# Kernel optimization log

Hardware: AMD Instinct MI355X
Metric: run time of the kernel (lower is better)

## Reference

```python
import jax, jax.numpy as jnp
import numpy as np

B, T, S, H, D = 2, 2048, 2048, 16, 64
E = H * D  # embed_dim = 1024


def setup_inputs() -> dict:
    key = jax.random.key(0)
    k1, k2, k3, k4 = jax.random.split(key, 4)
    q = jax.random.normal(k1, (B, T, H, D), jnp.float32)
    kv = jax.random.normal(k2, (B, S, 2, H, D), jnp.float32)
    # nn.MultiheadAttention packed in-projection (xavier-ish scale) and out-projection
    in_proj_w = jax.random.normal(k3, (3 * E, E), jnp.float32) * (1.0 / np.sqrt(E)).astype(np.float32)
    in_proj_b = jnp.zeros((3 * E,), jnp.float32)
    out_proj_w = jax.random.normal(k4, (E, E), jnp.float32) * (1.0 / np.sqrt(E)).astype(np.float32)
    out_proj_b = jnp.zeros((E,), jnp.float32)
    return {"q": q, "kv": kv, "in_proj_w": in_proj_w, "in_proj_b": in_proj_b,
            "out_proj_w": out_proj_w, "out_proj_b": out_proj_b}


def reference(q, kv, in_proj_w, in_proj_b, out_proj_w, out_proj_b):
    Bq, Tq, Hh, Dd = q.shape
    Ss = kv.shape[1]
    Ee = Hh * Dd
    # flatten heads: q -> (B,T,E); kv unbinds k (two=0) and v (two=1)
    qf = q.reshape(Bq, Tq, Ee)
    kf = kv[:, :, 0].reshape(Bq, Ss, Ee)
    vf = kv[:, :, 1].reshape(Bq, Ss, Ee)
    wq, wk, wv = jnp.split(in_proj_w, 3, axis=0)
    bq, bk, bv = jnp.split(in_proj_b, 3)
    qp = (qf @ wq.T + bq).reshape(Bq, Tq, Hh, Dd).transpose(0, 2, 1, 3)  # bhtd
    kp = (kf @ wk.T + bk).reshape(Bq, Ss, Hh, Dd).transpose(0, 2, 1, 3)  # bhsd
    vp = (vf @ wv.T + bv).reshape(Bq, Ss, Hh, Dd).transpose(0, 2, 1, 3)  # bhsd
    scale = 1.0 / jnp.sqrt(jnp.asarray(Dd, qp.dtype))
    scores = jnp.einsum('bhtd,bhsd->bhts', qp, kp) * scale
    attn = jax.nn.softmax(scores, axis=-1)  # full SxS materialization, as in non-fused MHA
    ctx = jnp.einsum('bhts,bhsd->bhtd', attn, vp)
    ctx = ctx.transpose(0, 2, 1, 3).reshape(Bq, Tq, Ee)
    out = (ctx @ out_proj_w.T + out_proj_b).reshape(Bq, Tq, Hh, Dd)
    # need_weights=True default: weights averaged over heads -> (B,T,S)
    attn_weights = attn.mean(axis=1)
    return out, attn_weights
```

## Files before the change

kernel.cpp:

```cpp
#include <hip/hip_runtime.h>
#include <math.h>

#define Bb 2
#define Tt 2048
#define Ssz 2048
#define Hh 16
#define Dd 64
#define Ee 1024

#define NQ  (Bb*Tt*Ee)
#define NKV (Bb*Ssz*Ee)
#define NW  (3*Ee*Ee)
#define NWO (Ee*Ee)

#define LOG2E 1.44269504088896f

typedef __bf16 bf16x8 __attribute__((ext_vector_type(8)));
typedef float  floatx4 __attribute__((ext_vector_type(4)));
typedef unsigned short u16;
typedef unsigned int   u32;

__device__ __forceinline__ u16 f2bf(float f) {
    __bf16 h = (__bf16)f;
    union { __bf16 h; u16 u; } v; v.h = h; return v.u;
}
__device__ __forceinline__ float bf2f(u16 b) {
    union { u32 u; float f; } v; v.u = ((u32)b) << 16; return v.f;
}
__device__ __forceinline__ float load_f(const void* p, int i, bool isbf) {
    if (isbf) return bf2f(((const u16*)p)[i]);
    return ((const float*)p)[i];
}
__device__ __forceinline__ u32 load2(const void* p, int i, bool isbf) {
    if (isbf) return ((const u32*)p)[i >> 1];
    float2 f = ((const float2*)p)[i >> 1];
    return (u32)f2bf(f.x) | ((u32)f2bf(f.y) << 16);
}

typedef __attribute__((address_space(1))) const unsigned int gas_u32;
typedef __attribute__((address_space(3))) unsigned int las_u32;
__device__ __forceinline__ void gl_lds16(const u16* g, u16* l) {
    __builtin_amdgcn_global_load_lds((gas_u32*)g, (las_u32*)l, 16, 0, 0);
}

__device__ __forceinline__ int swz(int k, int row) {
    return (k & ~63) | ((((k >> 3) ^ row) & 7) << 3) | (k & 7);
}

__global__ void k_detect(const u32* __restrict__ qw, int* __restrict__ flag) {
    __shared__ int cnt;
    if (threadIdx.x == 0) cnt = 0;
    __syncthreads();
    int h = 0;
    for (int i = threadIdx.x; i < 4096; i += 256) {
        u32 w = qw[i];
        u32 b = (w >> 8) & 0x7Fu;
        if ((b & 0x7Cu) == 0x3Cu) h++;
    }
    atomicAdd(&cnt, h);
    __syncthreads();
    if (threadIdx.x == 0) flag[0] = (cnt > 2048) ? 1 : 0;
}

__global__ void k_pack(const void* __restrict__ q, const void* __restrict__ kv,
                       const void* __restrict__ w_in, const void* __restrict__ b_in,
                       const void* __restrict__ w_out, const void* __restrict__ b_out,
                       const int* __restrict__ flag,
                       u32* __restrict__ qb, u32* __restrict__ kb, u32* __restrict__ vb,
                       u32* __restrict__ wb, u32* __restrict__ wob, float* __restrict__ biases) {
    bool isbf = flag[0] != 0;
    int i = (blockIdx.x * 256 + threadIdx.x) * 2;
    if (i < NQ) { int row = i >> 10, k = i & 1023;
        qb[(((size_t)row << 10) | (u32)swz(k, row)) >> 1] = load2(q, i, isbf); return; }
    i -= NQ;
    if (i < NKV) { int row = i >> 10, e = i & 1023;
        kb[(((size_t)row << 10) | (u32)swz(e, row)) >> 1] = load2(kv, row*2048 + e, isbf); return; }
    i -= NKV;
    if (i < NKV) { int row = i >> 10, e = i & 1023;
        vb[(((size_t)row << 10) | (u32)swz(e, row)) >> 1] = load2(kv, row*2048 + 1024 + e, isbf); return; }
    i -= NKV;
    if (i < NW) { int row = i >> 10, k = i & 1023;
        wb[(((size_t)row << 10) | (u32)swz(k, row)) >> 1] = load2(w_in, i, isbf); return; }
    i -= NW;
    if (i < NWO) { int row = i >> 10, k = i & 1023;
        wob[(((size_t)row << 10) | (u32)swz(k, row)) >> 1] = load2(w_out, i, isbf); return; }
    i -= NWO;
    if (i < 3072) { biases[i] = load_f(b_in, i, isbf); biases[i+1] = load_f(b_in, i+1, isbf); return; }
    i -= 3072;
    if (i < 1024) { biases[3072+i] = load_f(b_out, i, isbf); biases[3072+i+1] = load_f(b_out, i+1, isbf); }
}

__device__ __forceinline__ void gemm128(const u16* __restrict__ Ab, const u16* __restrict__ Wb,
                                        u16* As, u16* Ws, floatx4 (&acc)[4][4], int tid) {
    int lane = tid & 63, w = tid >> 6, q = lane >> 4, ml = lane & 15;
    int mh = (w >> 1) * 64, nh = (w & 1) * 64;
    int rs = tid >> 3, cs = (tid & 7) * 8;
    for (int k0 = 0; k0 < 1024; k0 += 64) {
        __syncthreads();
#pragma unroll
        for (int j = 0; j < 4; ++j)
            gl_lds16(Ab + (size_t)(j*32 + rs) * 1024 + k0 + cs, &As[(j*32 + rs)*64 + cs]);
#pragma unroll
        for (int j = 0; j < 4; ++j)
            gl_lds16(Wb + (size_t)(j*32 + rs) * 1024 + k0 + cs, &Ws[(j*32 + rs)*64 + cs]);
        __syncthreads();
#pragma unroll
        for (int kk = 0; kk < 2; ++kk) {
            int gs = (((kk*4 + q) ^ ml) & 7) * 8;
            bf16x8 af[4], bfv[4];
#pragma unroll
            for (int mt = 0; mt < 4; ++mt) af[mt]  = *(const bf16x8*)&As[(mh + mt*16 + ml)*64 + gs];
#pragma unroll
            for (int nt = 0; nt < 4; ++nt) bfv[nt] = *(const bf16x8*)&Ws[(nh + nt*16 + ml)*64 + gs];
#pragma unroll
            for (int mt = 0; mt < 4; ++mt)
#pragma unroll
                for (int nt = 0; nt < 4; ++nt)
                    acc[mt][nt] = __builtin_amdgcn_mfma_f32_16x16x32_bf16(af[mt], bfv[nt], acc[mt][nt], 0, 0, 0);
        }
    }
}

__global__ __launch_bounds__(256) void k_gemm_qkv(const u16* __restrict__ qb, const u16* __restrict__ kb,
                                                  const u16* __restrict__ vb, const u16* __restrict__ wb,
                                                  const float* __restrict__ biases,
                                                  u16* __restrict__ Qp, u16* __restrict__ Kp,
                                                  u16* __restrict__ Vt) {
    __shared__ u16 As[128 * 64];
    __shared__ u16 Ws[128 * 64];
    int mode = blockIdx.z;
    const u16* A = (mode == 0) ? qb : (mode == 1) ? kb : vb;
    const u16* W = wb + (size_t)mode * Ee * Ee;
    const float* bias = biases + mode * 1024;
    int n0 = blockIdx.x * 128, m0 = blockIdx.y * 128;
    int tid = threadIdx.x, lane = tid & 63;
    int w = tid >> 6, q = lane >> 4, ml = lane & 15;
    int mh = (w >> 1) * 64, nh = (w & 1) * 64;

    floatx4 acc[4][4];
#pragma unroll
    for (int a = 0; a < 4; ++a)
#pragma unroll
        for (int b2 = 0; b2 < 4; ++b2) acc[a][b2] = (floatx4){0.f, 0.f, 0.f, 0.f};

    gemm128(A + (size_t)m0 * 1024, W + (size_t)n0 * 1024, As, Ws, acc, tid);

#pragma unroll
    for (int mt = 0; mt < 4; ++mt) {
#pragma unroll
        for (int nt = 0; nt < 4; ++nt) {
#pragma unroll
            for (int rg = 0; rg < 4; ++rg) {
                int m = m0 + mh + mt*16 + q*4 + rg;
                int n = n0 + nh + nt*16 + ml;
                float val = acc[mt][nt][rg] + bias[n];
                int b = m >> 11, t = m & 2047, hh = n >> 6, d = n & 63;
                if (mode == 0) {
                    int dsw = ((((d >> 3) ^ t) & 7) << 3) | (d & 7);
                    Qp[((size_t)(b*16 + hh) * 2048 + t) * 64 + dsw] = f2bf(val * (0.125f * LOG2E));
                } else if (mode == 1) {
                    int dsw = ((((d >> 3) ^ t) & 7) << 3) | (d & 7);
                    Kp[((size_t)(b*16 + hh) * 2048 + t) * 64 + dsw] = f2bf(val);
                } else {
                    int tsw = (t & ~63) | ((((t >> 3) ^ d) & 7) << 3) | (t & 7);
                    Vt[((size_t)(b*16 + hh) * 64 + d) * 2048 + tsw] = f2bf(val);
                }
            }
        }
    }
}

__global__ __launch_bounds__(256) void k_gemm_out(const u16* __restrict__ A, const u16* __restrict__ W,
                                                  const float* __restrict__ bias, void* __restrict__ Cout,
                                                  const int* __restrict__ flag) {
    __shared__ u16 As[128 * 64];
    __shared__ u16 Ws[128 * 64];
    int n0 = blockIdx.x * 128, m0 = blockIdx.y * 128;
    int tid = threadIdx.x, lane = tid & 63;
    int w = tid >> 6, q = lane >> 4, ml = lane & 15;
    int mh = (w >> 1) * 64, nh = (w & 1) * 64;

    floatx4 acc[4][4];
#pragma unroll
    for (int a = 0; a < 4; ++a)
#pragma unroll
        for (int b2 = 0; b2 < 4; ++b2) acc[a][b2] = (floatx4){0.f, 0.f, 0.f, 0.f};

    gemm128(A + (size_t)m0 * 1024, W + (size_t)n0 * 1024, As, Ws, acc, tid);

    bool outbf = flag[0] != 0;
#pragma unroll
    for (int mt = 0; mt < 4; ++mt) {
#pragma unroll
        for (int nt = 0; nt < 4; ++nt) {
#pragma unroll
            for (int rg = 0; rg < 4; ++rg) {
                int m = m0 + mh + mt*16 + q*4 + rg;
                int n = n0 + nh + nt*16 + ml;
                float val = acc[mt][nt][rg] + bias[n];
                if (outbf) ((u16*)Cout)[(size_t)m * 1024 + n] = f2bf(val);
                else       ((float*)Cout)[(size_t)m * 1024 + n] = val;
            }
        }
    }
}

__global__ __launch_bounds__(256) void k_flash(const u16* __restrict__ Qp, const u16* __restrict__ Kp,
                                               const u16* __restrict__ Vt, u16* __restrict__ ctx,
                                               float* __restrict__ lbuf) {
    __shared__ u16 Qs[128 * 64];
    __shared__ u16 Ks[64 * 64];
    __shared__ u16 Vs[64 * 64];
    __shared__ u16 Ps[128 * 64];
    int t0 = blockIdx.x * 128;
    int h  = blockIdx.y;
    int b  = blockIdx.z;
    const u16* Qh = Qp + (size_t)(b*16 + h) * 2048 * 64;
    const u16* Kh = Kp + (size_t)(b*16 + h) * 2048 * 64;
    const u16* Vh = Vt + (size_t)(b*16 + h) * 64 * 2048;
    int tid = threadIdx.x, lane = tid & 63;
    int w = tid >> 6, q = lane >> 4, ml = lane & 15;
    int rsw = tid >> 3, cs = (tid & 7) * 8;

#pragma unroll
    for (int j = 0; j < 4; ++j)
        gl_lds16(Qh + (size_t)(t0 + j*32 + rsw) * 64 + cs, &Qs[(j*32 + rsw)*64 + cs]);
    __syncthreads();

    bf16x8 qf[2][2];
#pragma unroll
    for (int mt = 0; mt < 2; ++mt)
#pragma unroll
        for (int kk = 0; kk < 2; ++kk)
            qf[mt][kk] = *(const bf16x8*)&Qs[(mt*64 + w*16 + ml)*64 + (((kk*4 + q) ^ ml) & 7)*8];

    float lp[2][4] = {{0.f,0.f,0.f,0.f},{0.f,0.f,0.f,0.f}};
    floatx4 ct[2][4];
#pragma unroll
    for (int mt = 0; mt < 2; ++mt)
#pragma unroll
        for (int i = 0; i < 4; ++i) ct[mt][i] = (floatx4){0.f, 0.f, 0.f, 0.f};

    for (int s0 = 0; s0 < 2048; s0 += 64) {
        __syncthreads();
#pragma unroll
        for (int j = 0; j < 2; ++j) {
            gl_lds16(Kh + (size_t)(s0 + j*32 + rsw) * 64 + cs, &Ks[(j*32 + rsw)*64 + cs]);
            gl_lds16(Vh + (size_t)(j*32 + rsw) * 2048 + s0 + cs, &Vs[(j*32 + rsw)*64 + cs]);
        }
        __syncthreads();

#pragma unroll
        for (int mt = 0; mt < 2; ++mt) {
            floatx4 sc[4];
#pragma unroll
            for (int i = 0; i < 4; ++i) sc[i] = (floatx4){0.f, 0.f, 0.f, 0.f};
#pragma unroll
            for (int kk = 0; kk < 2; ++kk) {
                int gs = (((kk*4 + q) ^ ml) & 7) * 8;
#pragma unroll
                for (int nt = 0; nt < 4; ++nt) {
                    bf16x8 kf = *(const bf16x8*)&Ks[(nt*16 + ml)*64 + gs];
                    sc[nt] = __builtin_amdgcn_mfma_f32_16x16x32_bf16(qf[mt][kk], kf, sc[nt], 0, 0, 0);
                }
            }
#pragma unroll
            for (int nt = 0; nt < 4; ++nt) {
#pragma unroll
                for (int rg = 0; rg < 4; ++rg) {
                    float p = __builtin_amdgcn_exp2f(sc[nt][rg]);
                    lp[mt][rg] += p;
                    int rr = q*4 + rg;
                    Ps[(mt*64 + w*16 + rr)*64 + (((nt*2 + (ml >> 3)) ^ rr) & 7)*8 + (ml & 7)] = f2bf(p);
                }
            }
        }

#pragma unroll
        for (int kk = 0; kk < 2; ++kk) {
            int gs = (((kk*4 + q) ^ ml) & 7) * 8;
            bf16x8 pf0 = *(const bf16x8*)&Ps[(w*16 + ml)*64 + gs];
            bf16x8 pf1 = *(const bf16x8*)&Ps[(64 + w*16 + ml)*64 + gs];
#pragma unroll
            for (int nt = 0; nt < 4; ++nt) {
                bf16x8 vf = *(const bf16x8*)&Vs[(nt*16 + ml)*64 + gs];
                ct[0][nt] = __builtin_amdgcn_mfma_f32_16x16x32_bf16(pf0, vf, ct[0][nt], 0, 0, 0);
                ct[1][nt] = __builtin_amdgcn_mfma_f32_16x16x32_bf16(pf1, vf, ct[1][nt], 0, 0, 0);
            }
        }
    }

#pragma unroll
    for (int mt = 0; mt < 2; ++mt)
#pragma unroll
        for (int rg = 0; rg < 4; ++rg)
#pragma unroll
            for (int off = 1; off < 16; off <<= 1) lp[mt][rg] += __shfl_xor(lp[mt][rg], off, 16);
    if (ml == 0) {
#pragma unroll
        for (int mt = 0; mt < 2; ++mt) {
            size_t base = (size_t)(b*16 + h) * 2048 + t0 + mt*64 + w*16 + q*4;
#pragma unroll
            for (int rg = 0; rg < 4; ++rg) lbuf[base + rg] = lp[mt][rg];
        }
    }

#pragma unroll
    for (int mt = 0; mt < 2; ++mt) {
        float il[4];
#pragma unroll
        for (int rg = 0; rg < 4; ++rg) il[rg] = 1.f / lp[mt][rg];
#pragma unroll
        for (int nt = 0; nt < 4; ++nt) {
#pragma unroll
            for (int rg = 0; rg < 4; ++rg) {
                int t = t0 + mt*64 + w*16 + q*4 + rg;
                int c64 = nt*16 + ml;
                int col = h*64 + (((((c64 >> 3) ^ t) & 7)) << 3) + (c64 & 7);
                ctx[(size_t)(b*2048 + t) * 1024 + col] = f2bf(ct[mt][nt][rg] * il[rg]);
            }
        }
    }
}

__global__ __launch_bounds__(256) void k_attnw(const u16* __restrict__ Qp, const u16* __restrict__ Kp,
                                               const float* __restrict__ lbuf,
                                               void* __restrict__ dout, const int* __restrict__ flag) {
    __shared__ u16 Qs[64 * 64];
    __shared__ u16 Ks[128 * 64];
    int s0 = blockIdx.x * 128;
    int t0 = blockIdx.y * 64;
    int b  = blockIdx.z;
    int tid = threadIdx.x, lane = tid & 63;
    int w = tid >> 6, q = lane >> 4, ml = lane & 15;
    int rsw = tid >> 3, cs = (tid & 7) * 8;

    floatx4 aw[8];
#pragma unroll
    for (int i = 0; i < 8; ++i) aw[i] = (floatx4){0.f, 0.f, 0.f, 0.f};

    for (int h = 0; h < 16; ++h) {
        const u16* Qh = Qp + (size_t)(b*16 + h) * 2048 * 64;
        const u16* Kh = Kp + (size_t)(b*16 + h) * 2048 * 64;
        __syncthreads();
#pragma unroll
        for (int j = 0; j < 2; ++j)
            gl_lds16(Qh + (size_t)(t0 + j*32 + rsw) * 64 + cs, &Qs[(j*32 + rsw)*64 + cs]);
#pragma unroll
        for (int j = 0; j < 4; ++j)
            gl_lds16(Kh + (size_t)(s0 + j*32 + rsw) * 64 + cs, &Ks[(j*32 + rsw)*64 + cs]);
        __syncthreads();

        float il[4];
        size_t sb = (size_t)(b*16 + h) * 2048 + t0 + w*16 + q*4;
#pragma unroll
        for (int rg = 0; rg < 4; ++rg) il[rg] = 1.f / lbuf[sb + rg];

        floatx4 sc[8];
#pragma unroll
        for (int i = 0; i < 8; ++i) sc[i] = (floatx4){0.f, 0.f, 0.f, 0.f};
#pragma unroll
        for (int kk = 0; kk < 2; ++kk) {
            int gs = (((kk*4 + q) ^ ml) & 7) * 8;
            bf16x8 qfr = *(const bf16x8*)&Qs[(w*16 + ml)*64 + gs];
#pragma unroll
            for (int nt = 0; nt < 8; ++nt) {
                bf16x8 kfr = *(const bf16x8*)&Ks[(nt*16 + ml)*64 + gs];
                sc[nt] = __builtin_amdgcn_mfma_f32_16x16x32_bf16(qfr, kfr, sc[nt], 0, 0, 0);
            }
        }
#pragma unroll
        for (int nt = 0; nt < 8; ++nt)
#pragma unroll
            for (int rg = 0; rg < 4; ++rg)
                aw[nt][rg] += __builtin_amdgcn_exp2f(sc[nt][rg]) * il[rg];
    }

    bool outbf = flag[0] != 0;
    const size_t attn_base = (size_t)Bb * Tt * Ee;
#pragma unroll
    for (int nt = 0; nt < 8; ++nt) {
#pragma unroll
        for (int rg = 0; rg < 4; ++rg) {
            int t = t0 + w*16 + q*4 + rg;
            int s = s0 + nt*16 + ml;
            float val = aw[nt][rg] * 0.0625f;
            size_t idx = attn_base + (size_t)(b*2048 + t) * 2048 + s;
            if (outbf) ((u16*)dout)[idx] = f2bf(val);
            else       ((float*)dout)[idx] = val;
        }
    }
}

extern "C" void kernel_launch(void* const* d_in, const int* in_sizes, int n_in,
                              void* d_out, int out_size, void* d_ws, size_t ws_size,
                              hipStream_t stream) {
    const void* q     = d_in[0];
    const void* kv    = d_in[1];
    const void* w_in  = d_in[2];
    const void* b_in  = d_in[3];
    const void* w_out = d_in[4];
    const void* b_out = d_in[5];

    char* ws = (char*)d_ws;
    size_t off = 0;
    auto alloc = [&](size_t bytes) -> void* {
        void* p = ws + off;
        off += (bytes + 255) & ~(size_t)255;
        return p;
    };
    int*   flag   = (int*)alloc(256);
    u16*   qb     = (u16*)alloc((size_t)NQ * 2);
    u16*   kb     = (u16*)alloc((size_t)NKV * 2);
    u16*   vb     = (u16*)alloc((size_t)NKV * 2);
    u16*   wb     = (u16*)alloc((size_t)NW * 2);
    u16*   wob    = (u16*)alloc((size_t)NWO * 2);
    float* biases = (float*)alloc(4096 * 4);
    u16*   Qp     = (u16*)alloc((size_t)NQ * 2);
    u16*   Kp     = (u16*)alloc((size_t)NKV * 2);
    u16*   Vt     = (u16*)alloc((size_t)NKV * 2);
    u16*   ctx    = (u16*)alloc((size_t)NQ * 2);
    float* lbuf   = (float*)alloc((size_t)Bb * Hh * Tt * 4);

    k_detect<<<1, 256, 0, stream>>>((const u32*)q, flag);

    int totalPairs = (NQ + NKV + NKV + NW + NWO + 4096) / 2;
    k_pack<<<(totalPairs + 255) / 256, 256, 0, stream>>>(q, kv, w_in, b_in, w_out, b_out, flag,
                                                         (u32*)qb, (u32*)kb, (u32*)vb,
                                                         (u32*)wb, (u32*)wob, biases);

    k_gemm_qkv<<<dim3(8, 32, 3), 256, 0, stream>>>(qb, kb, vb, wb, biases, Qp, Kp, Vt);

    k_flash<<<dim3(Tt / 128, Hh, Bb), 256, 0, stream>>>(Qp, Kp, Vt, ctx, lbuf);
    k_attnw<<<dim3(Ssz / 128, Tt / 64, Bb), 256, 0, stream>>>(Qp, Kp, lbuf, d_out, flag);

    k_gemm_out<<<dim3(8, 32), 256, 0, stream>>>(ctx, wob, biases + 3072, d_out, flag);
}
```

Before: 313.6 us.

## Restructure flash kernel with double-buffered K/V, register P, split-S waves; remap GEMM grids

The flash attention kernel goes to 512 threads. Waves split the key range into two halves, and the partial context and row sums are reduced through LDS at the end. K and V tiles are double-buffered so the next tile's loads overlap compute, which removes one barrier per iteration. Scores are computed transposed so P stays in registers and feeds a 16x16x16 MFMA directly instead of round-tripping through LDS. The QKV and output GEMMs also remap block indices so neighbouring blocks spread across the XCDs, in exchange for extra index math and reduction overhead.

```diff
diff --git a/kernel.cpp b/kernel.cpp
--- a/kernel.cpp
+++ b/kernel.cpp
@@ -17,6 +17,7 @@
 
 typedef __bf16 bf16x8 __attribute__((ext_vector_type(8)));
 typedef float  floatx4 __attribute__((ext_vector_type(4)));
+typedef short  short4_ __attribute__((ext_vector_type(4)));
 typedef unsigned short u16;
 typedef unsigned int   u32;
 
@@ -128,11 +129,15 @@
                                                   u16* __restrict__ Vt) {
     __shared__ u16 As[128 * 64];
     __shared__ u16 Ws[128 * 64];
-    int mode = blockIdx.z;
+    int flat = blockIdx.x + 8 * (blockIdx.y + 32 * blockIdx.z);
+    int wg = (flat & 7) * 96 + (flat >> 3);
+    int mode = wg >> 8;
+    int rem = wg & 255;
+    int m0 = (rem >> 3) * 128;
+    int n0 = (rem & 7) * 128;
     const u16* A = (mode == 0) ? qb : (mode == 1) ? kb : vb;
     const u16* W = wb + (size_t)mode * Ee * Ee;
     const float* bias = biases + mode * 1024;
-    int n0 = blockIdx.x * 128, m0 = blockIdx.y * 128;
     int tid = threadIdx.x, lane = tid & 63;
     int w = tid >> 6, q = lane >> 4, ml = lane & 15;
     int mh = (w >> 1) * 64, nh = (w & 1) * 64;
@@ -175,7 +180,10 @@
                                                   const int* __restrict__ flag) {
     __shared__ u16 As[128 * 64];
     __shared__ u16 Ws[128 * 64];
-    int n0 = blockIdx.x * 128, m0 = blockIdx.y * 128;
+    int flat = blockIdx.x + 8 * blockIdx.y;
+    int wg = (flat & 7) * 32 + (flat >> 3);
+    int m0 = (wg >> 3) * 128;
+    int n0 = (wg & 7) * 128;
     int tid = threadIdx.x, lane = tid & 63;
     int w = tid >> 6, q = lane >> 4, ml = lane & 15;
     int mh = (w >> 1) * 64, nh = (w & 1) * 64;
@@ -205,13 +213,13 @@
     }
 }
 
-__global__ __launch_bounds__(256) void k_flash(const u16* __restrict__ Qp, const u16* __restrict__ Kp,
+__global__ __launch_bounds__(512) void k_flash(const u16* __restrict__ Qp, const u16* __restrict__ Kp,
                                                const u16* __restrict__ Vt, u16* __restrict__ ctx,
                                                float* __restrict__ lbuf) {
-    __shared__ u16 Qs[128 * 64];
-    __shared__ u16 Ks[64 * 64];
-    __shared__ u16 Vs[64 * 64];
-    __shared__ u16 Ps[128 * 64];
+    __shared__ u16 smem[3 * 64 * 128];
+    u16* Qs = smem;
+    u16* KsB = smem + 8192;
+    u16* VsB = smem + 16384;
     int t0 = blockIdx.x * 128;
     int h  = blockIdx.y;
     int b  = blockIdx.z;
@@ -219,12 +227,15 @@
     const u16* Kh = Kp + (size_t)(b*16 + h) * 2048 * 64;
     const u16* Vh = Vt + (size_t)(b*16 + h) * 64 * 2048;
     int tid = threadIdx.x, lane = tid & 63;
-    int w = tid >> 6, q = lane >> 4, ml = lane & 15;
+    int wv = tid >> 6, r = wv & 3, e = wv >> 2;
+    int q = lane >> 4, ml = lane & 15;
     int rsw = tid >> 3, cs = (tid & 7) * 8;
 
 #pragma unroll
-    for (int j = 0; j < 4; ++j)
-        gl_lds16(Qh + (size_t)(t0 + j*32 + rsw) * 64 + cs, &Qs[(j*32 + rsw)*64 + cs]);
+    for (int j = 0; j < 2; ++j)
+        gl_lds16(Qh + (size_t)(t0 + j*64 + rsw) * 64 + cs, &Qs[(j*64 + rsw)*64 + cs]);
+    gl_lds16(Kh + (size_t)rsw * 64 + cs, &KsB[rsw*64 + cs]);
+    gl_lds16(Vh + (size_t)rsw * 2048 + cs, &VsB[rsw*64 + cs]);
     __syncthreads();
 
     bf16x8 qf[2][2];
@@ -232,92 +243,124 @@
     for (int mt = 0; mt < 2; ++mt)
 #pragma unroll
         for (int kk = 0; kk < 2; ++kk)
-            qf[mt][kk] = *(const bf16x8*)&Qs[(mt*64 + w*16 + ml)*64 + (((kk*4 + q) ^ ml) & 7)*8];
-
-    float lp[2][4] = {{0.f,0.f,0.f,0.f},{0.f,0.f,0.f,0.f}};
+            qf[mt][kk] = *(const bf16x8*)&Qs[(r*32 + mt*16 + ml)*64 + (((kk*4 + q) ^ ml) & 7)*8];
+
+    float lp[2] = {0.f, 0.f};
     floatx4 ct[2][4];
 #pragma unroll
     for (int mt = 0; mt < 2; ++mt)
 #pragma unroll
         for (int i = 0; i < 4; ++i) ct[mt][i] = (floatx4){0.f, 0.f, 0.f, 0.f};
 
+    int cur = 0;
     for (int s0 = 0; s0 < 2048; s0 += 64) {
-        __syncthreads();
-#pragma unroll
-        for (int j = 0; j < 2; ++j) {
-            gl_lds16(Kh + (size_t)(s0 + j*32 + rsw) * 64 + cs, &Ks[(j*32 + rsw)*64 + cs]);
-            gl_lds16(Vh + (size_t)(j*32 + rsw) * 2048 + s0 + cs, &Vs[(j*32 + rsw)*64 + cs]);
-        }
-        __syncthreads();
-
-#pragma unroll
-        for (int mt = 0; mt < 2; ++mt) {
-            floatx4 sc[4];
-#pragma unroll
-            for (int i = 0; i < 4; ++i) sc[i] = (floatx4){0.f, 0.f, 0.f, 0.f};
-#pragma unroll
-            for (int kk = 0; kk < 2; ++kk) {
-                int gs = (((kk*4 + q) ^ ml) & 7) * 8;
-#pragma unroll
-                for (int nt = 0; nt < 4; ++nt) {
-                    bf16x8 kf = *(const bf16x8*)&Ks[(nt*16 + ml)*64 + gs];
-                    sc[nt] = __builtin_amdgcn_mfma_f32_16x16x32_bf16(qf[mt][kk], kf, sc[nt], 0, 0, 0);
-                }
-            }
-#pragma unroll
-            for (int nt = 0; nt < 4; ++nt) {
-#pragma unroll
-                for (int rg = 0; rg < 4; ++rg) {
-                    float p = __builtin_amdgcn_exp2f(sc[nt][rg]);
-                    lp[mt][rg] += p;
-                    int rr = q*4 + rg;
-                    Ps[(mt*64 + w*16 + rr)*64 + (((nt*2 + (ml >> 3)) ^ rr) & 7)*8 + (ml & 7)] = f2bf(p);
-                }
-            }
-        }
-
+        if (s0 + 64 < 2048) {
+            gl_lds16(Kh + (size_t)(s0 + 64 + rsw) * 64 + cs, &KsB[(cur ^ 1)*4096 + rsw*64 + cs]);
+            gl_lds16(Vh + (size_t)rsw * 2048 + (s0 + 64) + cs, &VsB[(cur ^ 1)*4096 + rsw*64 + cs]);
+        }
+        const u16* Ksc = KsB + cur*4096;
+        const u16* Vsc = VsB + cur*4096;
+
+        floatx4 sc[2][2];
+#pragma unroll
+        for (int mt = 0; mt < 2; ++mt)
+#pragma unroll
+            for (int i = 0; i < 2; ++i) sc[mt][i] = (floatx4){0.f, 0.f, 0.f, 0.f};
 #pragma unroll
         for (int kk = 0; kk < 2; ++kk) {
             int gs = (((kk*4 + q) ^ ml) & 7) * 8;
-            bf16x8 pf0 = *(const bf16x8*)&Ps[(w*16 + ml)*64 + gs];
-            bf16x8 pf1 = *(const bf16x8*)&Ps[(64 + w*16 + ml)*64 + gs];
+#pragma unroll
+            for (int ntl = 0; ntl < 2; ++ntl) {
+                bf16x8 kf = *(const bf16x8*)&Ksc[(e*32 + ntl*16 + ml)*64 + gs];
+#pragma unroll
+                for (int mt = 0; mt < 2; ++mt)
+                    sc[mt][ntl] = __builtin_amdgcn_mfma_f32_16x16x32_bf16(kf, qf[mt][kk], sc[mt][ntl], 0, 0, 0);
+            }
+        }
+
+        short4_ pa[2][2];
+#pragma unroll
+        for (int mt = 0; mt < 2; ++mt) {
+#pragma unroll
+            for (int ntl = 0; ntl < 2; ++ntl) {
+#pragma unroll
+                for (int rg = 0; rg < 4; ++rg) {
+                    float p = __builtin_amdgcn_exp2f(sc[mt][ntl][rg]);
+                    lp[mt] += p;
+                    pa[mt][ntl][rg] = (short)f2bf(p);
+                }
+            }
+        }
+
+#pragma unroll
+        for (int ksl = 0; ksl < 2; ++ksl) {
 #pragma unroll
             for (int nt = 0; nt < 4; ++nt) {
-                bf16x8 vf = *(const bf16x8*)&Vs[(nt*16 + ml)*64 + gs];
-                ct[0][nt] = __builtin_amdgcn_mfma_f32_16x16x32_bf16(pf0, vf, ct[0][nt], 0, 0, 0);
-                ct[1][nt] = __builtin_amdgcn_mfma_f32_16x16x32_bf16(pf1, vf, ct[1][nt], 0, 0, 0);
-            }
-        }
-    }
-
-#pragma unroll
-    for (int mt = 0; mt < 2; ++mt)
-#pragma unroll
-        for (int rg = 0; rg < 4; ++rg)
-#pragma unroll
-            for (int off = 1; off < 16; off <<= 1) lp[mt][rg] += __shfl_xor(lp[mt][rg], off, 16);
-    if (ml == 0) {
+                const u16* vp = &Vsc[(nt*16 + ml)*64
+                                     + (((((e*2 + ksl)*2 + (q >> 1)) ^ ml) & 7) << 3) + (q & 1)*4];
+                short4_ vf = *(const short4_*)vp;
+#pragma unroll
+                for (int mt = 0; mt < 2; ++mt)
+                    ct[mt][nt] = __builtin_amdgcn_mfma_f32_16x16x16bf16_1k(pa[mt][ksl], vf, ct[mt][nt], 0, 0, 0);
+            }
+        }
+
+        __syncthreads();
+        cur ^= 1;
+    }
+
+#pragma unroll
+    for (int mt = 0; mt < 2; ++mt) {
+        lp[mt] += __shfl_xor(lp[mt], 16);
+        lp[mt] += __shfl_xor(lp[mt], 32);
+    }
+
+    float* redc = (float*)(smem + 8192);
+    float* redl = (float*)smem;
+    int basec = r*2048 + lane*32;
+    if (e == 1) {
+#pragma unroll
+        for (int mt = 0; mt < 2; ++mt)
+#pragma unroll
+            for (int nt = 0; nt < 4; ++nt) {
+                int g = mt*4 + nt;
+                *(floatx4*)&redc[basec + ((g ^ (lane & 7)) << 2)] = ct[mt][nt];
+            }
+        redl[(r*64 + lane)*2]     = lp[0];
+        redl[(r*64 + lane)*2 + 1] = lp[1];
+    }
+    __syncthreads();
+    if (e == 0) {
+#pragma unroll
+        for (int mt = 0; mt < 2; ++mt)
+#pragma unroll
+            for (int nt = 0; nt < 4; ++nt) {
+                int g = mt*4 + nt;
+                ct[mt][nt] += *(const floatx4*)&redc[basec + ((g ^ (lane & 7)) << 2)];
+            }
+        lp[0] += redl[(r*64 + lane)*2];
+        lp[1] += redl[(r*64 + lane)*2 + 1];
+
+        if (lane < 16) {
+            size_t base = (size_t)(b*16 + h) * 2048 + t0 + r*32;
+#pragma unroll
+            for (int mt = 0; mt < 2; ++mt) lbuf[base + mt*16 + lane] = lp[mt];
+        }
+
 #pragma unroll
         for (int mt = 0; mt < 2; ++mt) {
-            size_t base = (size_t)(b*16 + h) * 2048 + t0 + mt*64 + w*16 + q*4;
-#pragma unroll
-            for (int rg = 0; rg < 4; ++rg) lbuf[base + rg] = lp[mt][rg];
-        }
-    }
-
-#pragma unroll
-    for (int mt = 0; mt < 2; ++mt) {
-        float il[4];
-#pragma unroll
-        for (int rg = 0; rg < 4; ++rg) il[rg] = 1.f / lp[mt][rg];
-#pragma unroll
-        for (int nt = 0; nt < 4; ++nt) {
-#pragma unroll
-            for (int rg = 0; rg < 4; ++rg) {
-                int t = t0 + mt*64 + w*16 + q*4 + rg;
-                int c64 = nt*16 + ml;
-                int col = h*64 + (((((c64 >> 3) ^ t) & 7)) << 3) + (c64 & 7);
-                ctx[(size_t)(b*2048 + t) * 1024 + col] = f2bf(ct[mt][nt][rg] * il[rg]);
+            float il[4];
+#pragma unroll
+            for (int rg = 0; rg < 4; ++rg) il[rg] = 1.f / __shfl(lp[mt], q*4 + rg);
+#pragma unroll
+            for (int nt = 0; nt < 4; ++nt) {
+#pragma unroll
+                for (int rg = 0; rg < 4; ++rg) {
+                    int t = t0 + r*32 + mt*16 + q*4 + rg;
+                    int c64 = nt*16 + ml;
+                    int col = h*64 + (((((c64 >> 3) ^ t) & 7)) << 3) + (c64 & 7);
+                    ctx[(size_t)(b*2048 + t) * 1024 + col] = f2bf(ct[mt][nt][rg] * il[rg]);
+                }
             }
         }
     }
@@ -431,7 +474,7 @@
 
     k_gemm_qkv<<<dim3(8, 32, 3), 256, 0, stream>>>(qb, kb, vb, wb, biases, Qp, Kp, Vt);
 
-    k_flash<<<dim3(Tt / 128, Hh, Bb), 256, 0, stream>>>(Qp, Kp, Vt, ctx, lbuf);
+    k_flash<<<dim3(Tt / 128, Hh, Bb), 512, 0, stream>>>(Qp, Kp, Vt, ctx, lbuf);
     k_attnw<<<dim3(Ssz / 128, Tt / 64, Bb), 256, 0, stream>>>(Qp, Kp, lbuf, d_out, flag);
 
     k_gemm_out<<<dim3(8, 32), 256, 0, stream>>>(ctx, wob, biases + 3072, d_out, flag);
```

After: 286.5 us. 1.09x faster.
